# Kernel tuning notes

Measured on AMD Instinct MI355X. Metric: run time of the kernel, lower is better.

## Reference

```python
import jax, jax.numpy as jnp
import numpy as np


def setup_inputs() -> dict:
    key = jax.random.key(0)
    k1, k2 = jax.random.split(key)
    B, C, H, W = 8, 19, 512, 1024
    inputs = jax.random.normal(k1, (B, C, H, W), dtype=jnp.float32)
    targets = jax.random.randint(k2, (B, H, W), 0, C, dtype=jnp.int32)
    return {"inputs": inputs, "targets": targets}


def reference(inputs, targets):
    # inputs: [B, C, H, W] logits; targets: [B, H, W] int class ids
    C = inputs.shape[1]
    logp = jax.nn.log_softmax(inputs, axis=1)            # [B, C, H, W]
    t = targets.reshape(-1)                              # [N]
    # per-class inverse-frequency weights via single-pass histogram
    counts = jnp.zeros((C,), dtype=jnp.float32).at[t].add(1.0)
    inv_freq = jnp.where(counts > 0, 1.0 / jnp.maximum(counts, 1.0), 1.0)  # [C]
    weight = inv_freq[t]                                 # [N]
    # gather log-prob of the target class per pixel
    logp_flat = jnp.transpose(logp, (0, 2, 3, 1)).reshape(-1, C)  # [N, C]
    nll = -jnp.take_along_axis(logp_flat, t[:, None], axis=1)[:, 0]  # [N]
    return jnp.sum(weight * nll) / jnp.sum(weight)
```

## Files before the change

### kernel.cpp

```cpp
#include <hip/hip_runtime.h>

#define NUM_C 19
#define HW_SHIFT 19
#define HW (1 << HW_SHIFT)
#define NPIX (8 * HW)
#define NGROUPS (NPIX / 4)
#define BLOCK 256
#define GPT 2
#define NBLOCKS (NGROUPS / (BLOCK * GPT))


__global__ __launch_bounds__(BLOCK, 4) void ifl_main(const float* __restrict__ x,
                                                     const int* __restrict__ tgt,
                                                     float* __restrict__ ws) {
    __shared__ float red[2 * NUM_C];
    if (threadIdx.x < 2 * NUM_C) red[threadIdx.x] = 0.0f;
    __syncthreads();

    const int tid = blockIdx.x * BLOCK + threadIdx.x;
    const int p   = (tid * GPT) << 2;
    const int b   = p >> HW_SHIFT;
    const int r   = p & (HW - 1);
    const float* base = x + (((size_t)b * NUM_C) << HW_SHIFT) + r;

    const int4 t0 = *reinterpret_cast<const int4*>(tgt + p);
    const int4 t1 = *reinterpret_cast<const int4*>(tgt + p + 4);
    const int tg[8] = {t0.x, t0.y, t0.z, t0.w, t1.x, t1.y, t1.z, t1.w};

    float s[8], xt[8];
#pragma unroll
    for (int k = 0; k < 8; ++k) { s[k] = 0.0f; xt[k] = 0.0f; }

#pragma unroll
    for (int c = 0; c < NUM_C; ++c) {
        const float4 va = *reinterpret_cast<const float4*>(base + ((size_t)c << HW_SHIFT));
        const float4 vb = *reinterpret_cast<const float4*>(base + ((size_t)c << HW_SHIFT) + 4);
        const float v[8] = {va.x, va.y, va.z, va.w, vb.x, vb.y, vb.z, vb.w};
#pragma unroll
        for (int k = 0; k < 8; ++k) {
            s[k] += __expf(v[k]);
            xt[k] = (tg[k] == c) ? v[k] : xt[k];
        }
    }

    float acc[NUM_C], cnt[NUM_C];
#pragma unroll
    for (int c = 0; c < NUM_C; ++c) { acc[c] = 0.0f; cnt[c] = 0.0f; }

#pragma unroll
    for (int k = 0; k < 8; ++k) {
        const float nll = __logf(s[k]) - xt[k];
#pragma unroll
        for (int c = 0; c < NUM_C; ++c) {
            const bool h = (tg[k] == c);
            acc[c] += h ? nll : 0.0f;
            cnt[c] += h ? 1.0f : 0.0f;
        }
    }

#pragma unroll
    for (int c = 0; c < NUM_C; ++c) {
        float a = acc[c];
        float n = cnt[c];
#pragma unroll
        for (int off = 32; off > 0; off >>= 1) {
            a += __shfl_down(a, off, 64);
            n += __shfl_down(n, off, 64);
        }
        if ((threadIdx.x & 63) == 0) {
            atomicAdd(&red[c], a);
            atomicAdd(&red[NUM_C + c], n);
        }
    }
    __syncthreads();

    if (threadIdx.x < 2 * NUM_C) atomicAdd(&ws[threadIdx.x], red[threadIdx.x]);
}

__global__ void ifl_final(const float* __restrict__ ws, float* __restrict__ out) {
    if (threadIdx.x == 0) {
        float num = 0.0f, den = 0.0f;
#pragma unroll
        for (int c = 0; c < NUM_C; ++c) {
            const float cn = ws[NUM_C + c];
            const float inv = (cn > 0.0f) ? (1.0f / fmaxf(cn, 1.0f)) : 1.0f;
            num += inv * ws[c];
            den += inv * cn;
        }
        out[0] = num / den;
    }
}

extern "C" void kernel_launch(void* const* d_in, const int* in_sizes, int n_in,
                              void* d_out, int out_size, void* d_ws, size_t ws_size,
                              hipStream_t stream) {
    const float* x = (const float*)d_in[0];
    const int* tgt = (const int*)d_in[1];
    float* ws = (float*)d_ws;
    float* out = (float*)d_out;

    hipMemsetAsync(ws, 0, 2 * NUM_C * sizeof(float), stream);

    ifl_main<<<NBLOCKS, BLOCK, 0, stream>>>(x, tgt, ws);
    ifl_final<<<1, 64, 0, stream>>>(ws, out);
}
```

Baseline: 453.5 us.

## Use persistent grid with LDS histogram atomics and per-block partials

Replaces the one-shot grid with a fixed 2048-block grid where each thread loops over several 4-pixel groups. Per-pixel results now go straight into a shared-memory class histogram via LDS atomics, instead of a 19-class wave-shuffle reduction per thread. Each block writes its own partial slots, which a 256-thread final kernel sums, so the global atomics and the memset are gone. The goal is to cut reduction overhead and register pressure. The cost is LDS atomic contention across 19 bins and a bigger final reduction.

Result: no change. 451.8 us (-0.4%).

```diff
diff --git a/kernel.cpp b/kernel.cpp
--- a/kernel.cpp
+++ b/kernel.cpp
@@ -6,85 +6,92 @@
 #define NPIX (8 * HW)
 #define NGROUPS (NPIX / 4)
 #define BLOCK 256
-#define GPT 2
-#define NBLOCKS (NGROUPS / (BLOCK * GPT))
+#define GRID 2048
+#define NTH (GRID * BLOCK)
+#define SLOTS 40
 
-
-__global__ __launch_bounds__(BLOCK, 4) void ifl_main(const float* __restrict__ x,
-                                                     const int* __restrict__ tgt,
-                                                     float* __restrict__ ws) {
-    __shared__ float red[2 * NUM_C];
-    if (threadIdx.x < 2 * NUM_C) red[threadIdx.x] = 0.0f;
+__global__ __launch_bounds__(BLOCK) void ifl_main(const float* __restrict__ x,
+                                                  const int* __restrict__ tgt,
+                                                  float* __restrict__ part) {
+    __shared__ float red[SLOTS];
+    if (threadIdx.x < SLOTS) red[threadIdx.x] = 0.0f;
     __syncthreads();
 
     const int tid = blockIdx.x * BLOCK + threadIdx.x;
-    const int p   = (tid * GPT) << 2;
-    const int b   = p >> HW_SHIFT;
-    const int r   = p & (HW - 1);
-    const float* base = x + (((size_t)b * NUM_C) << HW_SHIFT) + r;
-
-    const int4 t0 = *reinterpret_cast<const int4*>(tgt + p);
-    const int4 t1 = *reinterpret_cast<const int4*>(tgt + p + 4);
-    const int tg[8] = {t0.x, t0.y, t0.z, t0.w, t1.x, t1.y, t1.z, t1.w};
-
-    float s[8], xt[8];
-#pragma unroll
-    for (int k = 0; k < 8; ++k) { s[k] = 0.0f; xt[k] = 0.0f; }
 
 #pragma unroll
-    for (int c = 0; c < NUM_C; ++c) {
-        const float4 va = *reinterpret_cast<const float4*>(base + ((size_t)c << HW_SHIFT));
-        const float4 vb = *reinterpret_cast<const float4*>(base + ((size_t)c << HW_SHIFT) + 4);
-        const float v[8] = {va.x, va.y, va.z, va.w, vb.x, vb.y, vb.z, vb.w};
+    for (int it = 0; it < NGROUPS / NTH; ++it) {
+        const int g = tid + it * NTH;
+        const int p = g << 2;
+        const int b = p >> HW_SHIFT;
+        const int r = p & (HW - 1);
+        const float* base = x + (((size_t)b * NUM_C) << HW_SHIFT) + r;
+
+        const int4 t4 = *reinterpret_cast<const int4*>(tgt + p);
+
+        float s0 = 0.f, s1 = 0.f, s2 = 0.f, s3 = 0.f;
+        float x0 = 0.f, x1 = 0.f, x2 = 0.f, x3 = 0.f;
 #pragma unroll
-        for (int k = 0; k < 8; ++k) {
-            s[k] += __expf(v[k]);
-            xt[k] = (tg[k] == c) ? v[k] : xt[k];
+        for (int c = 0; c < NUM_C; ++c) {
+            const float4 v = *reinterpret_cast<const float4*>(base + ((size_t)c << HW_SHIFT));
+            s0 += __expf(v.x); s1 += __expf(v.y); s2 += __expf(v.z); s3 += __expf(v.w);
+            x0 = (t4.x == c) ? v.x : x0;
+            x1 = (t4.y == c) ? v.y : x1;
+            x2 = (t4.z == c) ? v.z : x2;
+            x3 = (t4.w == c) ? v.w : x3;
         }
+        atomicAdd(&red[t4.x], __logf(s0) - x0);
+        atomicAdd(&red[t4.y], __logf(s1) - x1);
+        atomicAdd(&red[t4.z], __logf(s2) - x2);
+        atomicAdd(&red[t4.w], __logf(s3) - x3);
+        atomicAdd(&red[NUM_C + t4.x], 1.0f);
+        atomicAdd(&red[NUM_C + t4.y], 1.0f);
+        atomicAdd(&red[NUM_C + t4.z], 1.0f);
+        atomicAdd(&red[NUM_C + t4.w], 1.0f);
     }
 
-    float acc[NUM_C], cnt[NUM_C];
+    __syncthreads();
+    if (threadIdx.x < SLOTS) part[blockIdx.x * SLOTS + threadIdx.x] = red[threadIdx.x];
+}
+
+__global__ __launch_bounds__(BLOCK) void ifl_final(const float* __restrict__ part,
+                                                   float* __restrict__ out) {
+    __shared__ float red[SLOTS];
+    if (threadIdx.x < SLOTS) red[threadIdx.x] = 0.0f;
+    __syncthreads();
+
+    float acc[SLOTS];
 #pragma unroll
-    for (int c = 0; c < NUM_C; ++c) { acc[c] = 0.0f; cnt[c] = 0.0f; }
+    for (int s = 0; s < SLOTS; ++s) acc[s] = 0.0f;
 
+    for (int k = threadIdx.x; k < GRID; k += BLOCK) {
+        const float4* p4 = reinterpret_cast<const float4*>(part + (size_t)k * SLOTS);
 #pragma unroll
-    for (int k = 0; k < 8; ++k) {
-        const float nll = __logf(s[k]) - xt[k];
-#pragma unroll
-        for (int c = 0; c < NUM_C; ++c) {
-            const bool h = (tg[k] == c);
-            acc[c] += h ? nll : 0.0f;
-            cnt[c] += h ? 1.0f : 0.0f;
+        for (int q = 0; q < SLOTS / 4; ++q) {
+            const float4 v = p4[q];
+            acc[4 * q + 0] += v.x;
+            acc[4 * q + 1] += v.y;
+            acc[4 * q + 2] += v.z;
+            acc[4 * q + 3] += v.w;
         }
     }
 
 #pragma unroll
-    for (int c = 0; c < NUM_C; ++c) {
-        float a = acc[c];
-        float n = cnt[c];
+    for (int s = 0; s < SLOTS; ++s) {
+        float v = acc[s];
 #pragma unroll
-        for (int off = 32; off > 0; off >>= 1) {
-            a += __shfl_down(a, off, 64);
-            n += __shfl_down(n, off, 64);
-        }
-        if ((threadIdx.x & 63) == 0) {
-            atomicAdd(&red[c], a);
-            atomicAdd(&red[NUM_C + c], n);
-        }
+        for (int off = 32; off > 0; off >>= 1) v += __shfl_down(v, off, 64);
+        if ((threadIdx.x & 63) == 0) atomicAdd(&red[s], v);
     }
     __syncthreads();
 
-    if (threadIdx.x < 2 * NUM_C) atomicAdd(&ws[threadIdx.x], red[threadIdx.x]);
-}
-
-__global__ void ifl_final(const float* __restrict__ ws, float* __restrict__ out) {
     if (threadIdx.x == 0) {
-        float num = 0.0f, den = 0.0f;
+        float num = 0.f, den = 0.f;
 #pragma unroll
         for (int c = 0; c < NUM_C; ++c) {
-            const float cn = ws[NUM_C + c];
-            const float inv = (cn > 0.0f) ? (1.0f / fmaxf(cn, 1.0f)) : 1.0f;
-            num += inv * ws[c];
+            const float cn = red[NUM_C + c];
+            const float inv = (cn > 0.f) ? (1.f / fmaxf(cn, 1.f)) : 1.f;
+            num += inv * red[c];
             den += inv * cn;
         }
         out[0] = num / den;
@@ -99,8 +106,6 @@
     float* ws = (float*)d_ws;
     float* out = (float*)d_out;
 
-    hipMemsetAsync(ws, 0, 2 * NUM_C * sizeof(float), stream);
-
-    ifl_main<<<NBLOCKS, BLOCK, 0, stream>>>(x, tgt, ws);
-    ifl_final<<<1, 64, 0, stream>>>(ws, out);
+    ifl_main<<<GRID, BLOCK, 0, stream>>>(x, tgt, ws);
+    ifl_final<<<1, BLOCK, 0, stream>>>(ws, out);
 }
```
